# Optimization experiments

Measured on AMD Instinct MI355X. Metric: run time of the kernel, lower is better.

The kernel has to match this reference:

```python
import jax, jax.numpy as jnp
import numpy as np

N_NODES = 50000
N_EDGES = 800000
IN_DIM = 128
HID = 32
HEADS = 4
OUT_DIM = 64
NEG_SLOPE = 0.2  # DGL GATConv default


def setup_inputs() -> dict:
    key = jax.random.key(0)
    ks = jax.random.split(key, 20)

    def glorot(k, shape):
        fan = shape[0] + shape[-1]
        return (jax.random.normal(k, shape, jnp.float32) * np.sqrt(2.0 / fan)).astype(jnp.float32)

    inp = {
        "h": jax.random.normal(ks[0], (N_NODES, IN_DIM), jnp.float32),
        "src": jax.random.randint(ks[1], (N_EDGES,), 0, N_NODES, jnp.int32),
        "dst": jax.random.randint(ks[2], (N_EDGES,), 0, N_NODES, jnp.int32),
        # layer 0: in_dim -> hidden, HEADS heads, relu
        "W1": glorot(ks[3], (IN_DIM, HEADS * HID)),
        "al1": glorot(ks[4], (HEADS, HID)),
        "ar1": glorot(ks[5], (HEADS, HID)),
        "b1": jnp.zeros((HEADS * HID,), jnp.float32),
        # layer 1 (hidden): hidden*heads -> hidden, HEADS heads, relu
        "W2": glorot(ks[6], (HEADS * HID, HEADS * HID)),
        "al2": glorot(ks[7], (HEADS, HID)),
        "ar2": glorot(ks[8], (HEADS, HID)),
        "b2": jnp.zeros((HEADS * HID,), jnp.float32),
        # layer 2 (output): hidden*heads -> out_dim, 1 head, no activation
        "W3": glorot(ks[9], (HEADS * HID, OUT_DIM)),
        "al3": glorot(ks[10], (1, OUT_DIM)),
        "ar3": glorot(ks[11], (1, OUT_DIM)),
        "b3": jnp.zeros((OUT_DIM,), jnp.float32),
    }
    return inp


def gat_conv(h, src, dst, W, attn_l, attn_r, bias, heads, out_dim, use_relu):
    n = h.shape[0]
    feat = (h @ W).reshape(n, heads, out_dim)              # [N,H,D]
    el = jnp.sum(feat * attn_l[None], axis=-1)             # [N,H]
    er = jnp.sum(feat * attn_r[None], axis=-1)             # [N,H]
    e = jax.nn.leaky_relu(el[src] + er[dst], NEG_SLOPE)    # [E,H] per-edge logits
    # segment softmax over incoming edges of each dst node
    emax = jax.ops.segment_max(e, dst, num_segments=n)     # [N,H] (-inf for isolated nodes, never gathered)
    ee = jnp.exp(e - emax[dst])                            # [E,H]
    denom = jax.ops.segment_sum(ee, dst, num_segments=n)   # [N,H]
    alpha = ee / denom[dst]                                # [E,H]
    msg = feat[src] * alpha[:, :, None]                    # [E,H,D] gather + weight
    out = jax.ops.segment_sum(msg, dst, num_segments=n)    # [N,H,D] scatter-add
    out = out + bias.reshape(1, heads, out_dim)
    if use_relu:
        out = jax.nn.relu(out)
    return out.reshape(n, heads * out_dim)


def reference(h, src, dst, W1, al1, ar1, b1, W2, al2, ar2, b2, W3, al3, ar3, b3):
    # dropout is identity in eval mode
    h1 = gat_conv(h, src, dst, W1, al1, ar1, b1, HEADS, HID, True)
    h2 = gat_conv(h1, src, dst, W2, al2, ar2, b2, HEADS, HID, True)
    h3 = gat_conv(h2, src, dst, W3, al3, ar3, b3, 1, OUT_DIM, False)
    return h3
```

## Files before the change

kernel.cpp:

```cpp
#include <hip/hip_runtime.h>
#include <hip/hip_fp16.h>

#define NNODES 50000
#define NEDGES 800000

__device__ __forceinline__ float leaky(float x) { return x >= 0.f ? x : 0.2f * x; }

typedef _Float16 f16x8 __attribute__((ext_vector_type(8)));
typedef float f32x4 __attribute__((ext_vector_type(4)));

struct __align__(8)  half4v { __half2 h0, h1; };
struct __align__(16) half8v { __half2 h0, h1, h2, h3; };

template<int F, int H, bool FP16IN>
__global__ __launch_bounds__(256) void gemm_mfma_k(const void* __restrict__ Xv,
                                                   const float* __restrict__ W,
                                                   const float* __restrict__ al,
                                                   const float* __restrict__ ar,
                                                   __half* __restrict__ Yh,
                                                   float* __restrict__ el,
                                                   float* __restrict__ er, int n) {
    constexpr int K = 128;
    constexpr int ROWS = 64;
    constexpr int LDK = K + 8;
    constexpr int NT = F / 16;
    __shared__ __align__(16) __half Xs[ROWS * LDK];
    __shared__ __align__(16) __half Wt[F * LDK];

    const int tid = threadIdx.x;
    const int r0 = blockIdx.x * ROWS;

    if constexpr (FP16IN) {
        const __half* X = (const __half*)Xv;
        for (int i = tid; i < ROWS * (K / 8); i += 256) {
            int r = i >> 4, c8 = i & 15;
            int row = r0 + r;
            half8v v;
            __half2 z = __halves2half2(__float2half_rn(0.f), __float2half_rn(0.f));
            v.h0 = z; v.h1 = z; v.h2 = z; v.h3 = z;
            if (row < n) v = ((const half8v*)X)[(size_t)row * (K / 8) + c8];
            *(half8v*)&Xs[r * LDK + c8 * 8] = v;
        }
    } else {
        const float* X = (const float*)Xv;
        for (int i = tid; i < ROWS * (K / 4); i += 256) {
            int r = i >> 5, c4 = i & 31;
            int row = r0 + r;
            float4 v = (row < n) ? ((const float4*)X)[(size_t)row * (K / 4) + c4]
                                 : make_float4(0.f, 0.f, 0.f, 0.f);
            __half* d = &Xs[r * LDK + c4 * 4];
            d[0] = __float2half_rn(v.x); d[1] = __float2half_rn(v.y);
            d[2] = __float2half_rn(v.z); d[3] = __float2half_rn(v.w);
        }
    }
    for (int i = tid; i < K * (F / 4); i += 256) {
        int k = i / (F / 4), n4 = i % (F / 4);
        float4 v = ((const float4*)W)[i];
        int nn = n4 * 4;
        Wt[(nn + 0) * LDK + k] = __float2half_rn(v.x);
        Wt[(nn + 1) * LDK + k] = __float2half_rn(v.y);
        Wt[(nn + 2) * LDK + k] = __float2half_rn(v.z);
        Wt[(nn + 3) * LDK + k] = __float2half_rn(v.w);
    }
    __syncthreads();

    const int wv = tid >> 6, lane = tid & 63;
    const int cl = lane & 15, kg = lane >> 4;

    f32x4 acc[NT];
    #pragma unroll
    for (int t = 0; t < NT; t++) acc[t] = (f32x4){0.f, 0.f, 0.f, 0.f};

    #pragma unroll
    for (int ks = 0; ks < K / 32; ks++) {
        f16x8 a = *(const f16x8*)&Xs[(16 * wv + cl) * LDK + ks * 32 + kg * 8];
        #pragma unroll
        for (int t = 0; t < NT; t++) {
            f16x8 b = *(const f16x8*)&Wt[(16 * t + cl) * LDK + ks * 32 + kg * 8];
            acc[t] = __builtin_amdgcn_mfma_f32_16x16x32_f16(a, b, acc[t], 0, 0, 0);
        }
    }

    #pragma unroll
    for (int t = 0; t < NT; t++)
        #pragma unroll
        for (int j = 0; j < 4; j++) {
            int row = r0 + 16 * wv + 4 * kg + j;
            if (row < n) Yh[(size_t)row * F + 16 * t + cl] = __float2half_rn(acc[t][j]);
        }

    float alv[NT], arv[NT];
    #pragma unroll
    for (int t = 0; t < NT; t++) { alv[t] = al[16 * t + cl]; arv[t] = ar[16 * t + cl]; }

    if (H == 1) {
        float pl[4], pr[4];
        #pragma unroll
        for (int j = 0; j < 4; j++) {
            pl[j] = 0.f; pr[j] = 0.f;
            #pragma unroll
            for (int t = 0; t < NT; t++) { pl[j] += acc[t][j] * alv[t]; pr[j] += acc[t][j] * arv[t]; }
        }
        #pragma unroll
        for (int off = 1; off < 16; off <<= 1)
            #pragma unroll
            for (int j = 0; j < 4; j++) { pl[j] += __shfl_xor(pl[j], off); pr[j] += __shfl_xor(pr[j], off); }
        if (cl == 0)
            #pragma unroll
            for (int j = 0; j < 4; j++) {
                int row = r0 + 16 * wv + 4 * kg + j;
                if (row < n) { el[row] = pl[j]; er[row] = pr[j]; }
            }
    } else {
        float pl[4][4], pr[4][4];
        #pragma unroll
        for (int hh = 0; hh < 4; hh++)
            #pragma unroll
            for (int j = 0; j < 4; j++) {
                pl[hh][j] = acc[2 * hh][j] * alv[2 * hh] + acc[2 * hh + 1][j] * alv[2 * hh + 1];
                pr[hh][j] = acc[2 * hh][j] * arv[2 * hh] + acc[2 * hh + 1][j] * arv[2 * hh + 1];
            }
        #pragma unroll
        for (int off = 1; off < 16; off <<= 1)
            #pragma unroll
            for (int hh = 0; hh < 4; hh++)
                #pragma unroll
                for (int j = 0; j < 4; j++) {
                    pl[hh][j] += __shfl_xor(pl[hh][j], off);
                    pr[hh][j] += __shfl_xor(pr[hh][j], off);
                }
        if (cl == 0)
            #pragma unroll
            for (int j = 0; j < 4; j++) {
                int row = r0 + 16 * wv + 4 * kg + j;
                if (row < n)
                    #pragma unroll
                    for (int hh = 0; hh < 4; hh++) {
                        el[row * 4 + hh] = pl[hh][j];
                        er[row * 4 + hh] = pr[hh][j];
                    }
            }
    }
}

__global__ void zero_k(int* __restrict__ cnt, int n) {
    int i = blockIdx.x * blockDim.x + threadIdx.x;
    if (i < n) cnt[i] = 0;
}

__global__ void hist_k(const int* __restrict__ dst, int* __restrict__ cnt,
                       int* __restrict__ rank) {
    int e = blockIdx.x * blockDim.x + threadIdx.x;
    if (e < NEDGES) rank[e] = atomicAdd(&cnt[dst[e]], 1);
}

__global__ void scan_blk_k(const int* __restrict__ cnt, int* __restrict__ offs,
                           int* __restrict__ bsum, int n) {
    __shared__ int sm[256];
    int tid = threadIdx.x;
    int i = blockIdx.x * 256 + tid;
    int v = (i < n) ? cnt[i] : 0;
    sm[tid] = v;
    __syncthreads();
    for (int off = 1; off < 256; off <<= 1) {
        int t = (tid >= off) ? sm[tid - off] : 0;
        __syncthreads();
        sm[tid] += t;
        __syncthreads();
    }
    if (i < n) offs[i] = sm[tid] - v;
    if (tid == 255) bsum[blockIdx.x] = sm[255];
}

__global__ void scan_top_k(int* __restrict__ bsum, int nb) {
    __shared__ int sm[256];
    int tid = threadIdx.x;
    int v = (tid < nb) ? bsum[tid] : 0;
    sm[tid] = v;
    __syncthreads();
    for (int off = 1; off < 256; off <<= 1) {
        int t = (tid >= off) ? sm[tid - off] : 0;
        __syncthreads();
        sm[tid] += t;
        __syncthreads();
    }
    if (tid < nb) bsum[tid] = sm[tid] - v;
}

__global__ void scan_add_k(int* __restrict__ offs, const int* __restrict__ bsum, int n) {
    int i = blockIdx.x * 256 + threadIdx.x;
    if (i < n) offs[i] += bsum[blockIdx.x];
    if (i == 0) offs[n] = NEDGES;
}

__global__ void scatter_k(const int* __restrict__ src, const int* __restrict__ dst,
                          const int* __restrict__ rank, const int* __restrict__ offs,
                          int* __restrict__ esrc) {
    int e = blockIdx.x * blockDim.x + threadIdx.x;
    if (e < NEDGES) esrc[offs[dst[e]] + rank[e]] = src[e];
}

__global__ __launch_bounds__(256) void node_agg4_k(const int* __restrict__ offs,
                                                   const int* __restrict__ esrc,
                                                   const float* __restrict__ el,
                                                   const float* __restrict__ er,
                                                   const __half* __restrict__ feat,
                                                   const float* __restrict__ bias,
                                                   __half* __restrict__ out) {
    const int lane = threadIdx.x & 63;
    const int gw0 = (blockIdx.x * 256 + threadIdx.x) >> 6;
    const int NW = (gridDim.x * 256) >> 6;

    const int h  = lane & 3;
    const int q  = lane >> 4;
    const int cl = lane & 15;
    const int hd = cl >> 2;

    float4 ba, bb;
    ba = *(const float4*)&bias[8 * cl];
    bb = *(const float4*)&bias[8 * cl + 4];

    for (int wid = gw0; wid < NNODES; wid += NW) {
        int beg = offs[wid], end = offs[wid + 1];
        float erh = er[wid * 4 + h];

        float acc[8] = {0.f, 0.f, 0.f, 0.f, 0.f, 0.f, 0.f, 0.f};
        float dsum = 0.f;
        for (int base = beg; base < end; base += 16) {
            int rem = end - base;
            if (rem > 16) rem = 16;
            int sv = 0;
            if (lane < rem) sv = esrc[base + lane];
            int se = __shfl(sv, lane >> 2);
            float p = 0.f;
            if ((lane >> 2) < rem)
                p = __expf(leaky(el[se * 4 + h] + erh));
            dsum += p;
            #pragma unroll
            for (int e = 0; e < 16 && e < rem; e += 4) {
                int eidx = e + q;
                int s = __shfl(sv, eidx);
                float a = __shfl(p, eidx * 4 + hd);
                half8v hv = *(const half8v*)&feat[(size_t)s * 128 + 8 * cl];
                float2 f0 = __half22float2(hv.h0);
                float2 f1 = __half22float2(hv.h1);
                float2 f2 = __half22float2(hv.h2);
                float2 f3 = __half22float2(hv.h3);
                acc[0] += f0.x * a; acc[1] += f0.y * a;
                acc[2] += f1.x * a; acc[3] += f1.y * a;
                acc[4] += f2.x * a; acc[5] += f2.y * a;
                acc[6] += f3.x * a; acc[7] += f3.y * a;
            }
        }
        #pragma unroll
        for (int c = 0; c < 8; c++) {
            acc[c] += __shfl_xor(acc[c], 16);
            acc[c] += __shfl_xor(acc[c], 32);
        }
        #pragma unroll
        for (int off = 4; off < 64; off <<= 1) dsum += __shfl_xor(dsum, off);
        float dh = __shfl(dsum, hd);
        float inv = dh > 0.f ? 1.f / dh : 0.f;
        if (q == 0) {
            float v0 = fmaxf(acc[0] * inv + ba.x, 0.f), v1 = fmaxf(acc[1] * inv + ba.y, 0.f);
            float v2 = fmaxf(acc[2] * inv + ba.z, 0.f), v3 = fmaxf(acc[3] * inv + ba.w, 0.f);
            float v4 = fmaxf(acc[4] * inv + bb.x, 0.f), v5 = fmaxf(acc[5] * inv + bb.y, 0.f);
            float v6 = fmaxf(acc[6] * inv + bb.z, 0.f), v7 = fmaxf(acc[7] * inv + bb.w, 0.f);
            half8v hv;
            hv.h0 = __halves2half2(__float2half_rn(v0), __float2half_rn(v1));
            hv.h1 = __halves2half2(__float2half_rn(v2), __float2half_rn(v3));
            hv.h2 = __halves2half2(__float2half_rn(v4), __float2half_rn(v5));
            hv.h3 = __halves2half2(__float2half_rn(v6), __float2half_rn(v7));
            *(half8v*)&out[(size_t)wid * 128 + 8 * cl] = hv;
        }
    }
}

__global__ __launch_bounds__(256) void node_agg1_k(const int* __restrict__ offs,
                                                   const int* __restrict__ esrc,
                                                   const float* __restrict__ el,
                                                   const float* __restrict__ er,
                                                   const __half* __restrict__ feat,
                                                   const float* __restrict__ bias,
                                                   float* __restrict__ out) {
    const int lane = threadIdx.x & 63;
    const int gw0 = (blockIdx.x * 256 + threadIdx.x) >> 6;
    const int NW = (gridDim.x * 256) >> 6;

    const int q  = lane >> 4;
    const int cl = lane & 15;
    float4 b4 = *(const float4*)&bias[4 * cl];

    for (int wid = gw0; wid < NNODES; wid += NW) {
        int beg = offs[wid], end = offs[wid + 1];
        float erd = er[wid];

        float acc[4] = {0.f, 0.f, 0.f, 0.f};
        float dsum = 0.f;
        for (int base = beg; base < end; base += 64) {
            int rem = end - base;
            if (rem > 64) rem = 64;
            int sv = 0;
            float p = 0.f;
            if (lane < rem) {
                sv = esrc[base + lane];
                p = __expf(leaky(el[sv] + erd));
            }
            dsum += p;
            #pragma unroll 4
            for (int e = 0; e < rem; e += 4) {
                int eidx = e + q;
                int s = __shfl(sv, eidx);
                float a = __shfl(p, eidx);
                half4v hv = *(const half4v*)&feat[(size_t)s * 64 + 4 * cl];
                float2 f0 = __half22float2(hv.h0);
                float2 f1 = __half22float2(hv.h1);
                acc[0] += f0.x * a; acc[1] += f0.y * a;
                acc[2] += f1.x * a; acc[3] += f1.y * a;
            }
        }
        #pragma unroll
        for (int c = 0; c < 4; c++) {
            acc[c] += __shfl_xor(acc[c], 16);
            acc[c] += __shfl_xor(acc[c], 32);
        }
        #pragma unroll
        for (int off = 1; off < 64; off <<= 1) dsum += __shfl_xor(dsum, off);
        float inv = dsum > 0.f ? 1.f / dsum : 0.f;
        if (q == 0) {
            *(float4*)&out[(size_t)wid * 64 + 4 * cl] =
                make_float4(acc[0] * inv + b4.x, acc[1] * inv + b4.y,
                            acc[2] * inv + b4.z, acc[3] * inv + b4.w);
        }
    }
}

extern "C" void kernel_launch(void* const* d_in, const int* in_sizes, int n_in,
                              void* d_out, int out_size, void* d_ws, size_t ws_size,
                              hipStream_t stream) {
    const float* h   = (const float*)d_in[0];
    const int*   src = (const int*)d_in[1];
    const int*   dst = (const int*)d_in[2];
    const float* W1  = (const float*)d_in[3];
    const float* al1 = (const float*)d_in[4];
    const float* ar1 = (const float*)d_in[5];
    const float* b1  = (const float*)d_in[6];
    const float* W2  = (const float*)d_in[7];
    const float* al2 = (const float*)d_in[8];
    const float* ar2 = (const float*)d_in[9];
    const float* b2  = (const float*)d_in[10];
    const float* W3  = (const float*)d_in[11];
    const float* al3 = (const float*)d_in[12];
    const float* ar3 = (const float*)d_in[13];
    const float* b3  = (const float*)d_in[14];
    float* out = (float*)d_out;

    const int n = NNODES;
    __half* feat16 = (__half*)d_ws;
    __half* hbuf16 = feat16 + (size_t)n * 128;
    float*  el     = (float*)(hbuf16 + (size_t)n * 128);
    float*  er     = el + (size_t)n * 4;
    int*    cnt    = (int*)(er + (size_t)n * 4);
    int*    offs   = cnt + n;
    int*    esrc   = offs + (n + 1);
    int*    bsum   = esrc + NEDGES;
    int*    rank   = (int*)feat16;

    const int gemmBlocks = (n + 63) / 64;
    const int nBlk = (n + 255) / 256;
    const int eBlk = (NEDGES + 255) / 256;
    const int aggBlk = 2048;

    zero_k<<<nBlk, 256, 0, stream>>>(cnt, n);
    hist_k<<<eBlk, 256, 0, stream>>>(dst, cnt, rank);
    scan_blk_k<<<nBlk, 256, 0, stream>>>(cnt, offs, bsum, n);
    scan_top_k<<<1, 256, 0, stream>>>(bsum, nBlk);
    scan_add_k<<<nBlk, 256, 0, stream>>>(offs, bsum, n);
    scatter_k<<<eBlk, 256, 0, stream>>>(src, dst, rank, offs, esrc);

    gemm_mfma_k<128, 4, false><<<gemmBlocks, 256, 0, stream>>>(h, W1, al1, ar1, feat16, el, er, n);
    node_agg4_k<<<aggBlk, 256, 0, stream>>>(offs, esrc, el, er, feat16, b1, hbuf16);

    gemm_mfma_k<128, 4, true><<<gemmBlocks, 256, 0, stream>>>(hbuf16, W2, al2, ar2, feat16, el, er, n);
    node_agg4_k<<<aggBlk, 256, 0, stream>>>(offs, esrc, el, er, feat16, b2, hbuf16);

    gemm_mfma_k<64, 1, true><<<gemmBlocks, 256, 0, stream>>>(hbuf16, W3, al3, ar3, feat16, el, er, n);
    node_agg1_k<<<aggBlk, 256, 0, stream>>>(offs, esrc, el, er, feat16, b3, out);
}
```

Baseline: 233.3 us.

## Fuse edge histogram into first GEMM launch and merge scan kernels

```diff
diff --git a/kernel.cpp b/kernel.cpp
--- a/kernel.cpp
+++ b/kernel.cpp
@@ -3,6 +3,7 @@
 
 #define NNODES 50000
 #define NEDGES 800000
+#define HISTB 256
 
 __device__ __forceinline__ float leaky(float x) { return x >= 0.f ? x : 0.2f * x; }
 
@@ -12,18 +13,30 @@
 struct __align__(8)  half4v { __half2 h0, h1; };
 struct __align__(16) half8v { __half2 h0, h1, h2, h3; };
 
-template<int F, int H, bool FP16IN>
+template<int F, int H, bool FP16IN, bool DO_HIST>
 __global__ __launch_bounds__(256) void gemm_mfma_k(const void* __restrict__ Xv,
                                                    const float* __restrict__ W,
                                                    const float* __restrict__ al,
                                                    const float* __restrict__ ar,
                                                    __half* __restrict__ Yh,
                                                    float* __restrict__ el,
-                                                   float* __restrict__ er, int n) {
+                                                   float* __restrict__ er, int n,
+                                                   int nGemm,
+                                                   const int* __restrict__ dst,
+                                                   int* __restrict__ cnt,
+                                                   int* __restrict__ rank) {
     constexpr int K = 128;
     constexpr int ROWS = 64;
     constexpr int LDK = K + 8;
     constexpr int NT = F / 16;
+
+    if (DO_HIST && blockIdx.x >= nGemm) {
+        int b = blockIdx.x - nGemm;
+        for (int e = b * 256 + threadIdx.x; e < NEDGES; e += HISTB * 256)
+            rank[e] = atomicAdd(&cnt[dst[e]], 1);
+        return;
+    }
+
     __shared__ __align__(16) __half Xs[ROWS * LDK];
     __shared__ __align__(16) __half Wt[F * LDK];
 
@@ -141,17 +154,6 @@
                     }
             }
     }
-}
-
-__global__ void zero_k(int* __restrict__ cnt, int n) {
-    int i = blockIdx.x * blockDim.x + threadIdx.x;
-    if (i < n) cnt[i] = 0;
-}
-
-__global__ void hist_k(const int* __restrict__ dst, int* __restrict__ cnt,
-                       int* __restrict__ rank) {
-    int e = blockIdx.x * blockDim.x + threadIdx.x;
-    if (e < NEDGES) rank[e] = atomicAdd(&cnt[dst[e]], 1);
 }
 
 __global__ void scan_blk_k(const int* __restrict__ cnt, int* __restrict__ offs,
@@ -172,7 +174,8 @@
     if (tid == 255) bsum[blockIdx.x] = sm[255];
 }
 
-__global__ void scan_top_k(int* __restrict__ bsum, int nb) {
+__global__ void scan_addtop_k(int* __restrict__ offs, const int* __restrict__ bsum,
+                              int n, int nb) {
     __shared__ int sm[256];
     int tid = threadIdx.x;
     int v = (tid < nb) ? bsum[tid] : 0;
@@ -184,12 +187,9 @@
         sm[tid] += t;
         __syncthreads();
     }
-    if (tid < nb) bsum[tid] = sm[tid] - v;
-}
-
-__global__ void scan_add_k(int* __restrict__ offs, const int* __restrict__ bsum, int n) {
-    int i = blockIdx.x * 256 + threadIdx.x;
-    if (i < n) offs[i] += bsum[blockIdx.x];
+    int prefix = (blockIdx.x > 0) ? sm[blockIdx.x - 1] : 0;
+    int i = blockIdx.x * 256 + tid;
+    if (i < n) offs[i] += prefix;
     if (i == 0) offs[n] = NEDGES;
 }
 
@@ -216,9 +216,8 @@
     const int cl = lane & 15;
     const int hd = cl >> 2;
 
-    float4 ba, bb;
-    ba = *(const float4*)&bias[8 * cl];
-    bb = *(const float4*)&bias[8 * cl + 4];
+    float4 ba = *(const float4*)&bias[8 * cl];
+    float4 bb = *(const float4*)&bias[8 * cl + 4];
 
     for (int wid = gw0; wid < NNODES; wid += NW) {
         int beg = offs[wid], end = offs[wid + 1];
@@ -364,26 +363,29 @@
     int*    offs   = cnt + n;
     int*    esrc   = offs + (n + 1);
     int*    bsum   = esrc + NEDGES;
-    int*    rank   = (int*)feat16;
+    int*    rank   = bsum + 256;
 
     const int gemmBlocks = (n + 63) / 64;
     const int nBlk = (n + 255) / 256;
     const int eBlk = (NEDGES + 255) / 256;
     const int aggBlk = 2048;
 
-    zero_k<<<nBlk, 256, 0, stream>>>(cnt, n);
-    hist_k<<<eBlk, 256, 0, stream>>>(dst, cnt, rank);
+    hipMemsetAsync(cnt, 0, (size_t)n * sizeof(int), stream);
+
+    gemm_mfma_k<128, 4, false, true><<<gemmBlocks + HISTB, 256, 0, stream>>>(
+        h, W1, al1, ar1, feat16, el, er, n, gemmBlocks, dst, cnt, rank);
+
     scan_blk_k<<<nBlk, 256, 0, stream>>>(cnt, offs, bsum, n);
-    scan_top_k<<<1, 256, 0, stream>>>(bsum, nBlk);
-    scan_add_k<<<nBlk, 256, 0, stream>>>(offs, bsum, n);
+    scan_addtop_k<<<nBlk, 256, 0, stream>>>(offs, bsum, n, nBlk);
     scatter_k<<<eBlk, 256, 0, stream>>>(src, dst, rank, offs, esrc);
 
-    gemm_mfma_k<128, 4, false><<<gemmBlocks, 256, 0, stream>>>(h, W1, al1, ar1, feat16, el, er, n);
     node_agg4_k<<<aggBlk, 256, 0, stream>>>(offs, esrc, el, er, feat16, b1, hbuf16);
 
-    gemm_mfma_k<128, 4, true><<<gemmBlocks, 256, 0, stream>>>(hbuf16, W2, al2, ar2, feat16, el, er, n);
+    gemm_mfma_k<128, 4, true, false><<<gemmBlocks, 256, 0, stream>>>(
+        hbuf16, W2, al2, ar2, feat16, el, er, n, gemmBlocks, nullptr, nullptr, nullptr);
     node_agg4_k<<<aggBlk, 256, 0, stream>>>(offs, esrc, el, er, feat16, b2, hbuf16);
 
-    gemm_mfma_k<64, 1, true><<<gemmBlocks, 256, 0, stream>>>(hbuf16, W3, al3, ar3, feat16, el, er, n);
+    gemm_mfma_k<64, 1, true, false><<<gemmBlocks, 256, 0, stream>>>(
+        hbuf16, W3, al3, ar3, feat16, el, er, n, gemmBlocks, nullptr, nullptr, nullptr);
     node_agg1_k<<<aggBlk, 256, 0, stream>>>(offs, esrc, el, er, feat16, b3, out);
 }
```

New measurement: 222.1 us. -4.8%, faster.
